# Optimization experiments

Hardware: AMD Instinct MI355X
Metric: run time of the kernel (lower is better)

The kernel has to match this reference:

```python
import jax, jax.numpy as jnp
import numpy as np
from jax import lax

BETA = 0.1

def setup_inputs() -> dict:
    key = jax.random.key(0)
    k = jax.random.split(key, 6)
    B, T, H, V = 2, 1024, 1024, 64000
    return {
        "_input": jax.random.normal(k[0], (B, T, H), jnp.float32) * 0.02,
        "weight": jax.random.normal(k[1], (V, H), jnp.float32) * 0.02,
        "attention_mask": (jax.random.uniform(k[2], (B, T)) < 0.9).astype(jnp.float32),
        "rewards": jax.random.normal(k[3], (B,), jnp.float32),
        "ref_input": jax.random.normal(k[4], (B, T, H), jnp.float32) * 0.02,
        "ref_weight": jax.random.normal(k[5], (V, H), jnp.float32) * 0.02,
    }


def _grpo(log_probs, attention_mask, rewards, ref_log_probs, beta):
    # log_probs: [B,T,V]
    chosen = jnp.argmax(log_probs, axis=-1)  # [B,T] int
    tok_lp = jnp.take_along_axis(log_probs, chosen[..., None], axis=-1)[..., 0]  # [B,T]
    ref_tok_lp = lax.stop_gradient(
        jnp.take_along_axis(ref_log_probs, chosen[..., None], axis=-1)[..., 0]
    )
    adv = (rewards - rewards.mean()) / (jnp.std(rewards, ddof=1) + 1e-8)  # [B]
    ratio = jnp.exp(tok_lp - lax.stop_gradient(tok_lp))  # == 1 in fwd, grad-carrying
    policy_loss = -ratio * adv[:, None]
    d = ref_tok_lp - tok_lp
    kl = jnp.exp(d) - d - 1.0
    per_tok = (policy_loss + beta * kl) * attention_mask
    seqlen = jnp.clip(attention_mask.sum(axis=1), 1.0)
    loss = (per_tok.sum(axis=1) / seqlen).mean()
    metrics = (
        tok_lp.mean(),
        jnp.std(tok_lp, ddof=1),
        log_probs.mean(),
        (kl * attention_mask).sum(axis=1).mean() / attention_mask.sum(axis=1).mean(),
    )
    return loss, metrics


def reference(_input, weight, attention_mask, rewards, ref_input, ref_weight):
    logits = jnp.einsum("bth,vh->btv", _input, weight)
    log_probs = jax.nn.log_softmax(logits, axis=-1)
    ref_logits = jnp.einsum("bth,vh->btv", ref_input, ref_weight)
    ref_log_probs = lax.stop_gradient(jax.nn.log_softmax(ref_logits, axis=-1))
    loss, metrics = _grpo(log_probs, attention_mask, rewards, ref_log_probs, BETA)
    return (loss, *metrics)
```

## Files before the change

### kernel.cpp

```cpp
#include <hip/hip_runtime.h>
#include <math.h>

#define GRPO_BETA 0.1f

constexpr int BM = 128;
constexpr int BN = 256;

typedef __attribute__((ext_vector_type(4))) float   f32x4;
typedef __attribute__((ext_vector_type(8))) __bf16  bf16x8;

__device__ __forceinline__ float sexp_fast(float a) { return __expf(fminf(a, 0.f)); }
__device__ __forceinline__ float sexp(float a)      { return expf(fminf(a, 0.f)); }

__device__ __forceinline__ bf16x8 cvt8(float4 a, float4 b) {
  bf16x8 r;
  r[0] = (__bf16)a.x; r[1] = (__bf16)a.y; r[2] = (__bf16)a.z; r[3] = (__bf16)a.w;
  r[4] = (__bf16)b.x; r[5] = (__bf16)b.y; r[6] = (__bf16)b.z; r[7] = (__bf16)b.w;
  return r;
}

__device__ __forceinline__ void bar_lgkm() {
  asm volatile("s_waitcnt lgkmcnt(0)\n\ts_barrier" ::: "memory");
}

__device__ __forceinline__ void gload_lds16(const void* g, void* l) {
  __builtin_amdgcn_global_load_lds(
      (const __attribute__((address_space(1))) void*)g,
      (__attribute__((address_space(3))) void*)l, 16, 0, 0);
}

__global__ __launch_bounds__(256)
void cvt_bf16_kernel(const float* __restrict__ src, __bf16* __restrict__ dst,
                     long long n8)
{
  long long i = (long long)blockIdx.x * blockDim.x + threadIdx.x;
  const long long stride = (long long)gridDim.x * blockDim.x;
  for (; i < n8; i += stride) {
    const float4 a = *reinterpret_cast<const float4*>(src + i * 8);
    const float4 b = *reinterpret_cast<const float4*>(src + i * 8 + 4);
    *reinterpret_cast<bf16x8*>(dst + i * 8) = cvt8(a, b);
  }
}

template <bool CVT, bool FULL>
__global__ __launch_bounds__(512, 4)
void fused_gemm_reduce(const float* __restrict__ AfP, const float* __restrict__ WfP,
                       const float* __restrict__ AfR, const float* __restrict__ WfR,
                       const __bf16* __restrict__ AhP, const __bf16* __restrict__ WhP,
                       const __bf16* __restrict__ AhR, const __bf16* __restrict__ WhR,
                       float* __restrict__ partP, float* __restrict__ partR,
                       int M, int K, int V, int NC, int NL, int gx)
{
  __shared__ __align__(16) unsigned short lds_a[BM * 64];
  __shared__ __align__(16) unsigned short lds_w[BN * 64];
  __shared__ __align__(16) float4 lds_red[BM * 4];

  const int tid  = threadIdx.x;
  const int lane = tid & 63;
  const int wave = tid >> 6;
  const int wm   = wave >> 2;
  const int wn   = wave & 3;
  const int l15  = lane & 15;
  const int q    = lane >> 4;

  const int nb  = gridDim.x;
  int wl = blockIdx.x;
  if ((nb & 7) == 0) wl = (wl & 7) * (nb >> 3) + (wl >> 3);
  const bool isPol = (wl & 1) == 0;
  const int  w2    = wl >> 1;
  const int  bx    = w2 % gx;
  const int  chunk = w2 / gx;
  const int  row0  = bx * BM;

  const float*  Af = isPol ? AfP : AfR;
  const float*  Wf = isPol ? WfP : WfR;
  const __bf16* Ah = isPol ? AhP : AhR;
  const __bf16* Wh = isPol ? WhP : WhR;

  const int rsub = lane >> 3;
  const int srcg = ((lane & 7) ^ rsub) * 8;

  const int t3 = tid & 3;
  const int r4 = tid >> 2;
  const int stw = ((t3 * 16) ^ ((r4 & 7) << 4));
  const int sta = r4 * 128 + stw;
  const int aroF = min(row0 + r4, M - 1) * K + t3 * 8;

  const int swzr  = ((q * 16) ^ ((l15 & 7) << 4));
  const int aoff0 = (wm * 64 + l15) * 128 + swzr;
  const int woff0 = (wn * 64 + l15) * 128 + swzr;

  float rm = -INFINITY, rse = 0.f, rsum = 0.f;
  int   ridx = 0x7fffffff;

  for (int sub = 0; sub < NL; ++sub) {
    const int v0 = (chunk * NL + sub) * BN;
    if (v0 >= V) break;

    f32x4 acc[4][4];
#pragma unroll
    for (int i = 0; i < 4; ++i)
#pragma unroll
      for (int j = 0; j < 4; ++j) acc[i][j] = (f32x4){0.f, 0.f, 0.f, 0.f};

    if constexpr (!CVT) {
      const __bf16* asrc[2];
#pragma unroll
      for (int c = 0; c < 2; ++c) {
        const int r = (wave + c * 8) * 8 + rsub;
        asrc[c] = Ah + (size_t)min(row0 + r, M - 1) * K + srcg;
      }
      const __bf16* wsrc[4];
#pragma unroll
      for (int c = 0; c < 4; ++c) {
        const int r = (wave + c * 8) * 8 + rsub;
        wsrc[c] = Wh + (size_t)min(v0 + r, V - 1) * K + srcg;
      }

      for (int kt = 0; kt < K; kt += 64) {
        __syncthreads();
#pragma unroll
        for (int c = 0; c < 2; ++c)
          gload_lds16(asrc[c] + kt,
                      reinterpret_cast<char*>(lds_a) + (wave + c * 8) * 1024);
#pragma unroll
        for (int c = 0; c < 4; ++c)
          gload_lds16(wsrc[c] + kt,
                      reinterpret_cast<char*>(lds_w) + (wave + c * 8) * 1024);
        __syncthreads();

#pragma unroll
        for (int kh = 0; kh < 2; ++kh) {
          const int p = kh << 6;
          bf16x8 afr[4];
#pragma unroll
          for (int f = 0; f < 4; ++f)
            afr[f] = *reinterpret_cast<const bf16x8*>(
                reinterpret_cast<const char*>(lds_a) + (aoff0 ^ p) + f * 2048);
          __builtin_amdgcn_s_setprio(1);
#pragma unroll
          for (int fn = 0; fn < 4; ++fn) {
            bf16x8 wfr = *reinterpret_cast<const bf16x8*>(
                reinterpret_cast<const char*>(lds_w) + (woff0 ^ p) + fn * 2048);
#pragma unroll
            for (int fm = 0; fm < 4; ++fm)
              acc[fm][fn] = __builtin_amdgcn_mfma_f32_16x16x32_bf16(
                  afr[fm], wfr, acc[fm][fn], 0, 0, 0);
          }
          __builtin_amdgcn_s_setprio(0);
        }
      }
      __syncthreads();
    } else {
      const int NS = K / 32;
      int wro[2];
#pragma unroll
      for (int i = 0; i < 2; ++i)
        wro[i] = min(v0 + r4 + 128 * i, V - 1) * K + t3 * 8;

      float4 aF[2], wF[2][2];
      aF[0] = *reinterpret_cast<const float4*>(Af + aroF);
      aF[1] = *reinterpret_cast<const float4*>(Af + aroF + 4);
#pragma unroll
      for (int i = 0; i < 2; ++i) {
        wF[i][0] = *reinterpret_cast<const float4*>(Wf + wro[i]);
        wF[i][1] = *reinterpret_cast<const float4*>(Wf + wro[i] + 4);
      }
      *reinterpret_cast<bf16x8*>(reinterpret_cast<char*>(lds_a) + sta) = cvt8(aF[0], aF[1]);
#pragma unroll
      for (int i = 0; i < 2; ++i)
        *reinterpret_cast<bf16x8*>(reinterpret_cast<char*>(lds_w) + (r4 + 128 * i) * 128 + stw) =
            cvt8(wF[i][0], wF[i][1]);
      if (NS > 1) {
        aF[0] = *reinterpret_cast<const float4*>(Af + aroF + 32);
        aF[1] = *reinterpret_cast<const float4*>(Af + aroF + 32 + 4);
#pragma unroll
        for (int i = 0; i < 2; ++i) {
          wF[i][0] = *reinterpret_cast<const float4*>(Wf + wro[i] + 32);
          wF[i][1] = *reinterpret_cast<const float4*>(Wf + wro[i] + 32 + 4);
        }
      }
      bar_lgkm();

      for (int s = 0; s < NS; ++s) {
        const int p = (s & 1) << 6;
        bf16x8 afr[4];
#pragma unroll
        for (int f = 0; f < 4; ++f)
          afr[f] = *reinterpret_cast<const bf16x8*>(
              reinterpret_cast<const char*>(lds_a) + (aoff0 ^ p) + f * 2048);
        __builtin_amdgcn_s_setprio(1);
#pragma unroll
        for (int fn = 0; fn < 4; ++fn) {
          bf16x8 wfr = *reinterpret_cast<const bf16x8*>(
              reinterpret_cast<const char*>(lds_w) + (woff0 ^ p) + fn * 2048);
#pragma unroll
          for (int fm = 0; fm < 4; ++fm)
            acc[fm][fn] = __builtin_amdgcn_mfma_f32_16x16x32_bf16(
                afr[fm], wfr, acc[fm][fn], 0, 0, 0);
        }
        __builtin_amdgcn_s_setprio(0);

        if (s + 1 < NS) {
          const int p1 = ((s + 1) & 1) << 6;
          *reinterpret_cast<bf16x8*>(reinterpret_cast<char*>(lds_a) + (sta ^ p1)) =
              cvt8(aF[0], aF[1]);
#pragma unroll
          for (int i = 0; i < 2; ++i)
            *reinterpret_cast<bf16x8*>(
                reinterpret_cast<char*>(lds_w) + (((r4 + 128 * i) * 128 + stw) ^ p1)) =
                cvt8(wF[i][0], wF[i][1]);
          if (s + 2 < NS) {
            const int kf = (s + 2) * 32;
            aF[0] = *reinterpret_cast<const float4*>(Af + aroF + kf);
            aF[1] = *reinterpret_cast<const float4*>(Af + aroF + kf + 4);
#pragma unroll
            for (int i = 0; i < 2; ++i) {
              wF[i][0] = *reinterpret_cast<const float4*>(Wf + wro[i] + kf);
              wF[i][1] = *reinterpret_cast<const float4*>(Wf + wro[i] + kf + 4);
            }
          }
        }
        bar_lgkm();
      }
    }

#pragma unroll
    for (int fm = 0; fm < 4; ++fm) {
#pragma unroll
      for (int reg = 0; reg < 4; ++reg) {
        float lm = -INFINITY;
#pragma unroll
        for (int fn = 0; fn < 4; ++fn) {
          if (FULL || v0 + wn * 64 + fn * 16 + l15 < V)
            lm = fmaxf(lm, acc[fm][fn][reg]);
        }
#pragma unroll
        for (int d = 1; d < 16; d <<= 1) lm = fmaxf(lm, __shfl_xor(lm, d));
        float se = 0.f, sm = 0.f; int li = 0x7fffffff;
#pragma unroll
        for (int fn = 0; fn < 4; ++fn) {
          const int v = v0 + wn * 64 + fn * 16 + l15;
          if (FULL || v < V) {
            const float x = acc[fm][fn][reg];
            se += __expf(x - lm);
            if (isPol) {
              sm += x;
              if (x == lm) li = min(li, v);
            }
          }
        }
        if (isPol) {
#pragma unroll
          for (int d = 1; d < 16; d <<= 1) {
            se += __shfl_xor(se, d);
            sm += __shfl_xor(sm, d);
            li  = min(li, __shfl_xor(li, d));
          }
        } else {
#pragma unroll
          for (int d = 1; d < 16; d <<= 1) se += __shfl_xor(se, d);
        }
        if (l15 == 0) {
          const int row = wm * 64 + fm * 16 + q * 4 + reg;
          lds_red[row * 4 + wn] = make_float4(lm, se, sm, __int_as_float(li));
        }
      }
    }
    __syncthreads();

    if (tid < BM) {
      float4 p0 = lds_red[tid * 4];
      float m = p0.x, se = p0.y, sm = p0.z; int idx = __float_as_int(p0.w);
#pragma unroll
      for (int j = 1; j < 4; ++j) {
        const float4 t = lds_red[tid * 4 + j];
        const int ti = __float_as_int(t.w);
        const float nm = fmaxf(m, t.x);
        se = se * sexp_fast(m - nm) + t.y * sexp_fast(t.x - nm);
        if (isPol) {
          sm += t.z;
          if (t.x > m || (t.x == m && ti < idx)) idx = ti;
        }
        m = nm;
      }
      const float nm = fmaxf(rm, m);
      rse = rse * sexp_fast(rm - nm) + se * sexp_fast(m - nm);
      if (isPol) {
        rsum += sm;
        if (m > rm || (m == rm && idx < ridx)) ridx = idx;
      }
      rm = nm;
    }
    __syncthreads();
  }

  if (tid < BM) {
    const int row = row0 + tid;
    if (row < M) {
      if (isPol) {
        reinterpret_cast<float4*>(partP)[(size_t)row * NC + chunk] =
            make_float4(rm, rse, rsum, __int_as_float(ridx));
      } else {
        reinterpret_cast<float2*>(partR)[(size_t)row * NC + chunk] =
            make_float2(rm, rse);
      }
    }
  }
}

__global__ __launch_bounds__(256)
void combine_kernel(const float4* __restrict__ partP,
                    const float2* __restrict__ partR,
                    const float* __restrict__ refA,
                    const float* __restrict__ refW,
                    float4* __restrict__ rowtab,
                    int M, int K, int V, int NC)
{
  const int row = blockIdx.x;
  const int tid = threadIdx.x;

  __shared__ float redf[256];
  __shared__ int   redi[256];
  __shared__ float s_M, s_SE, s_SUM, s_Mr, s_SEr, s_dot;
  __shared__ int   s_idx;

  float m = -INFINITY, se = 0.f, sm = 0.f; int idx = 0x7fffffff;
  for (int i = tid; i < NC; i += 256) {
    float4 p = partP[(size_t)row * NC + i];
    int pi = __float_as_int(p.w);
    float nm = fmaxf(m, p.x);
    se = se * sexp(m - nm) + p.y * sexp(p.x - nm);
    if (p.x > m || (p.x == m && pi < idx)) idx = pi;
    m = nm;
    sm += p.z;
  }
  redf[tid] = m; redi[tid] = idx;
  __syncthreads();
  for (int s = 128; s > 0; s >>= 1) {
    if (tid < s) {
      float om = redf[tid + s]; int oi = redi[tid + s];
      if (om > redf[tid] || (om == redf[tid] && oi < redi[tid])) { redf[tid] = om; redi[tid] = oi; }
    }
    __syncthreads();
  }
  if (tid == 0) { s_M = redf[0]; s_idx = redi[0]; }
  __syncthreads();
  const float Mp = s_M; const int chosen = s_idx;

  float contrib = se * sexp(m - Mp);
  __syncthreads();
  redf[tid] = contrib; __syncthreads();
  for (int s = 128; s > 0; s >>= 1) { if (tid < s) redf[tid] += redf[tid + s]; __syncthreads(); }
  if (tid == 0) s_SE = redf[0];
  __syncthreads();
  redf[tid] = sm; __syncthreads();
  for (int s = 128; s > 0; s >>= 1) { if (tid < s) redf[tid] += redf[tid + s]; __syncthreads(); }
  if (tid == 0) s_SUM = redf[0];
  __syncthreads();

  float mr = -INFINITY, ser = 0.f;
  for (int i = tid; i < NC; i += 256) {
    float2 p = partR[(size_t)row * NC + i];
    float nm = fmaxf(mr, p.x);
    ser = ser * sexp(mr - nm) + p.y * sexp(p.x - nm);
    mr = nm;
  }
  redf[tid] = mr; __syncthreads();
  for (int s = 128; s > 0; s >>= 1) { if (tid < s) redf[tid] = fmaxf(redf[tid], redf[tid + s]); __syncthreads(); }
  if (tid == 0) s_Mr = redf[0];
  __syncthreads();
  const float Mr = s_Mr;
  float contribr = ser * sexp(mr - Mr);
  __syncthreads();
  redf[tid] = contribr; __syncthreads();
  for (int s = 128; s > 0; s >>= 1) { if (tid < s) redf[tid] += redf[tid + s]; __syncthreads(); }
  if (tid == 0) s_SEr = redf[0];
  __syncthreads();

  float dp = 0.f;
  const float* ar = refA + (size_t)row * K;
  const float* wr = refW + (size_t)chosen * K;
  for (int j = tid * 4; j < K; j += 256 * 4) {
    float4 x = *reinterpret_cast<const float4*>(ar + j);
    float4 y = *reinterpret_cast<const float4*>(wr + j);
    dp = fmaf(x.x, y.x, dp);
    dp = fmaf(x.y, y.y, dp);
    dp = fmaf(x.z, y.z, dp);
    dp = fmaf(x.w, y.w, dp);
  }
  __syncthreads();
  redf[tid] = dp; __syncthreads();
  for (int s = 128; s > 0; s >>= 1) { if (tid < s) redf[tid] += redf[tid + s]; __syncthreads(); }
  if (tid == 0) s_dot = redf[0];
  __syncthreads();

  if (tid == 0) {
    float lse     = Mp + logf(s_SE);
    float tok     = Mp - lse;
    float ref_lse = Mr + logf(s_SEr);
    float ref_tok = s_dot - ref_lse;
    float d  = ref_tok - tok;
    float kl = expm1f(d) - d;
    float rm3 = s_SUM / (float)V - lse;
    rowtab[row] = make_float4(tok, kl, rm3, 0.f);
  }
}

__global__ __launch_bounds__(256)
void final_kernel(const float4* __restrict__ rowtab,
                  const float* __restrict__ mask,
                  const float* __restrict__ rewards,
                  float* __restrict__ out,
                  int M, int B, int T)
{
  const int tid = threadIdx.x;
  __shared__ float redf[256];
  __shared__ float s_mean, s_m3, s_var;
  __shared__ float s_kl[16], s_cnt[16];

  float st = 0.f, sm3 = 0.f;
  for (int r = tid; r < M; r += 256) {
    float4 v = rowtab[r];
    st += v.x; sm3 += v.z;
  }
  redf[tid] = st; __syncthreads();
  for (int s = 128; s > 0; s >>= 1) { if (tid < s) redf[tid] += redf[tid + s]; __syncthreads(); }
  if (tid == 0) s_mean = redf[0] / (float)M;
  __syncthreads();
  redf[tid] = sm3; __syncthreads();
  for (int s = 128; s > 0; s >>= 1) { if (tid < s) redf[tid] += redf[tid + s]; __syncthreads(); }
  if (tid == 0) s_m3 = redf[0] / (float)M;
  __syncthreads();

  const float mean = s_mean;
  float sv = 0.f;
  for (int r = tid; r < M; r += 256) { float d = rowtab[r].x - mean; sv = fmaf(d, d, sv); }
  __syncthreads();
  redf[tid] = sv; __syncthreads();
  for (int s = 128; s > 0; s >>= 1) { if (tid < s) redf[tid] += redf[tid + s]; __syncthreads(); }
  if (tid == 0) s_var = redf[0];
  __syncthreads();

  const int nb = B < 16 ? B : 16;
  for (int b = 0; b < nb; ++b) {
    float lk = 0.f, lc = 0.f;
    for (int t = tid; t < T; t += 256) {
      int r = b * T + t;
      float mk = mask[r];
      lk = fmaf(rowtab[r].y, mk, lk);
      lc += mk;
    }
    __syncthreads();
    redf[tid] = lk; __syncthreads();
    for (int s = 128; s > 0; s >>= 1) { if (tid < s) redf[tid] += redf[tid + s]; __syncthreads(); }
    if (tid == 0) s_kl[b] = redf[0];
    __syncthreads();
    redf[tid] = lc; __syncthreads();
    for (int s = 128; s > 0; s >>= 1) { if (tid < s) redf[tid] += redf[tid + s]; __syncthreads(); }
    if (tid == 0) s_cnt[b] = redf[0];
    __syncthreads();
  }

  if (tid == 0) {
    float rmean = 0.f;
    for (int b = 0; b < B; ++b) rmean += rewards[b];
    rmean /= (float)B;
    float rv = 0.f;
    for (int b = 0; b < B; ++b) { float d = rewards[b] - rmean; rv += d * d; }
    float rstd = sqrtf(rv / (float)(B > 1 ? B - 1 : 1));

    float loss = 0.f, m4n = 0.f, m4d = 0.f;
    for (int b = 0; b < nb; ++b) {
      float adv  = (rewards[b] - rmean) / (rstd + 1e-8f);
      float cnt  = s_cnt[b];
      float seql = fmaxf(cnt, 1.0f);
      loss += (-adv * cnt + GRPO_BETA * s_kl[b]) / seql;
      m4n += s_kl[b];
      m4d += cnt;
    }
    loss /= (float)B;

    out[0] = loss;
    out[1] = s_mean;
    out[2] = sqrtf(s_var / (float)(M - 1));
    out[3] = s_m3;
    out[4] = m4n / m4d;
  }
}

extern "C" void kernel_launch(void* const* d_in, const int* in_sizes, int n_in,
                              void* d_out, int out_size, void* d_ws, size_t ws_size,
                              hipStream_t stream)
{
  if (n_in < 6) return;
  const float* A       = (const float*)d_in[0];
  const float* W       = (const float*)d_in[1];
  const float* mask    = (const float*)d_in[2];
  const float* rewards = (const float*)d_in[3];
  const float* rA      = (const float*)d_in[4];
  const float* rW      = (const float*)d_in[5];

  const int M = in_sizes[2];
  const int B = in_sizes[3];
  const int T = M / B;
  const int K = in_sizes[0] / M;
  const int V = in_sizes[1] / K;

  const int gx = (M + BM - 1) / BM;
  const bool full = (V % BN) == 0;

  const size_t aBytes = (size_t)M * K * sizeof(__bf16);
  const size_t wBytes = (size_t)V * K * sizeof(__bf16);
  auto partBytes = [&](int nl) -> size_t {
    int nc = (V + BN * nl - 1) / (BN * nl);
    return (size_t)M * nc * 16 + (size_t)M * nc * 8 + (size_t)M * 16;
  };

  int NL = 1;
  bool canPrep = false;
  if (K % 64 == 0) {
    for (int nl = 1; nl <= 1024; nl <<= 1) {
      size_t pb = (partBytes(nl) + 255) & ~(size_t)255;
      if (pb + 2 * aBytes + 2 * wBytes <= ws_size) { NL = nl; canPrep = true; break; }
    }
  }
  if (!canPrep) {
    NL = 1;
    while (partBytes(NL) > ws_size && NL < 1024) NL <<= 1;
  }
  const int NC = (V + BN * NL - 1) / (BN * NL);

  float* partP  = (float*)d_ws;
  float* partR  = partP + (size_t)M * NC * 4;
  float* rowtab = partR + (size_t)M * NC * 2;

  dim3 g1(2 * gx * NC), b1(512);

  if (canPrep) {
    size_t pb = (partBytes(NL) + 255) & ~(size_t)255;
    __bf16* Ab  = (__bf16*)((char*)d_ws + pb);
    __bf16* rAb = Ab  + (size_t)M * K;
    __bf16* Wb  = rAb + (size_t)M * K;
    __bf16* rWb = Wb  + (size_t)V * K;

    const long long nA8 = (long long)M * K / 8;
    const long long nW8 = (long long)V * K / 8;
    cvt_bf16_kernel<<<dim3(512),  dim3(256), 0, stream>>>(A,  Ab,  nA8);
    cvt_bf16_kernel<<<dim3(512),  dim3(256), 0, stream>>>(rA, rAb, nA8);
    cvt_bf16_kernel<<<dim3(2048), dim3(256), 0, stream>>>(W,  Wb,  nW8);
    cvt_bf16_kernel<<<dim3(2048), dim3(256), 0, stream>>>(rW, rWb, nW8);

    if (full) {
      fused_gemm_reduce<false, true ><<<g1, b1, 0, stream>>>(
          nullptr, nullptr, nullptr, nullptr, Ab, Wb, rAb, rWb,
          partP, partR, M, K, V, NC, NL, gx);
    } else {
      fused_gemm_reduce<false, false><<<g1, b1, 0, stream>>>(
          nullptr, nullptr, nullptr, nullptr, Ab, Wb, rAb, rWb,
          partP, partR, M, K, V, NC, NL, gx);
    }
  } else {
    if (full) {
      fused_gemm_reduce<true , true ><<<g1, b1, 0, stream>>>(
          A, W, rA, rW, nullptr, nullptr, nullptr, nullptr,
          partP, partR, M, K, V, NC, NL, gx);
    } else {
      fused_gemm_reduce<true , false><<<g1, b1, 0, stream>>>(
          A, W, rA, rW, nullptr, nullptr, nullptr, nullptr,
          partP, partR, M, K, V, NC, NL, gx);
    }
  }

  combine_kernel<<<dim3(M), dim3(256), 0, stream>>>(
      (const float4*)partP, (const float2*)partR, rA, rW, (float4*)rowtab, M, K, V, NC);
  final_kernel<<<dim3(1), dim3(256), 0, stream>>>(
      (const float4*)rowtab, mask, rewards, (float*)d_out, M, B, T);
}
```

Measured before the change: 877.8 us.

## Double-buffer LDS tiles with async global-to-LDS loads across K=32 steps

```diff
diff --git a/kernel.cpp b/kernel.cpp
--- a/kernel.cpp
+++ b/kernel.cpp
@@ -77,15 +77,22 @@
   const __bf16* Ah = isPol ? AhP : AhR;
   const __bf16* Wh = isPol ? WhP : WhR;
 
-  const int rsub = lane >> 3;
-  const int srcg = ((lane & 7) ^ rsub) * 8;
+  const int lrow = lane >> 2;
+  const int gsw  = ((lane & 3) ^ (lrow & 3)) * 8;
+  const __bf16* asrc = Ah ? Ah + (size_t)min(row0 + wave * 16 + lrow, M - 1) * K + gsw : nullptr;
+  char* adst = reinterpret_cast<char*>(lds_a) + wave * 1024;
+  char* wdst0 = reinterpret_cast<char*>(lds_w) + wave * 1024;
+  char* wdst1 = reinterpret_cast<char*>(lds_w) + (wave + 8) * 1024;
+
+  const int rswz   = ((q ^ (l15 & 3)) << 4);
+  const int a32off = (wm * 64 + l15) * 64 + rswz;
+  const int w32off = (wn * 64 + l15) * 64 + rswz;
 
   const int t3 = tid & 3;
   const int r4 = tid >> 2;
   const int stw = ((t3 * 16) ^ ((r4 & 7) << 4));
   const int sta = r4 * 128 + stw;
   const int aroF = min(row0 + r4, M - 1) * K + t3 * 8;
-
   const int swzr  = ((q * 16) ^ ((l15 & 7) << 4));
   const int aoff0 = (wm * 64 + l15) * 128 + swzr;
   const int woff0 = (wn * 64 + l15) * 128 + swzr;
@@ -104,53 +111,52 @@
       for (int j = 0; j < 4; ++j) acc[i][j] = (f32x4){0.f, 0.f, 0.f, 0.f};
 
     if constexpr (!CVT) {
-      const __bf16* asrc[2];
-#pragma unroll
-      for (int c = 0; c < 2; ++c) {
-        const int r = (wave + c * 8) * 8 + rsub;
-        asrc[c] = Ah + (size_t)min(row0 + r, M - 1) * K + srcg;
-      }
-      const __bf16* wsrc[4];
-#pragma unroll
-      for (int c = 0; c < 4; ++c) {
-        const int r = (wave + c * 8) * 8 + rsub;
-        wsrc[c] = Wh + (size_t)min(v0 + r, V - 1) * K + srcg;
-      }
-
-      for (int kt = 0; kt < K; kt += 64) {
-        __syncthreads();
-#pragma unroll
-        for (int c = 0; c < 2; ++c)
-          gload_lds16(asrc[c] + kt,
-                      reinterpret_cast<char*>(lds_a) + (wave + c * 8) * 1024);
-#pragma unroll
-        for (int c = 0; c < 4; ++c)
-          gload_lds16(wsrc[c] + kt,
-                      reinterpret_cast<char*>(lds_w) + (wave + c * 8) * 1024);
-        __syncthreads();
-
-#pragma unroll
-        for (int kh = 0; kh < 2; ++kh) {
-          const int p = kh << 6;
-          bf16x8 afr[4];
-#pragma unroll
-          for (int f = 0; f < 4; ++f)
-            afr[f] = *reinterpret_cast<const bf16x8*>(
-                reinterpret_cast<const char*>(lds_a) + (aoff0 ^ p) + f * 2048);
-          __builtin_amdgcn_s_setprio(1);
-#pragma unroll
-          for (int fn = 0; fn < 4; ++fn) {
-            bf16x8 wfr = *reinterpret_cast<const bf16x8*>(
-                reinterpret_cast<const char*>(lds_w) + (woff0 ^ p) + fn * 2048);
-#pragma unroll
-            for (int fm = 0; fm < 4; ++fm)
-              acc[fm][fn] = __builtin_amdgcn_mfma_f32_16x16x32_bf16(
-                  afr[fm], wfr, acc[fm][fn], 0, 0, 0);
-          }
-          __builtin_amdgcn_s_setprio(0);
-        }
-      }
-      __syncthreads();
+      const __bf16* wsrc0 = Wh + (size_t)min(v0 + wave * 16 + lrow, V - 1) * K + gsw;
+      const __bf16* wsrc1 = Wh + (size_t)min(v0 + (wave + 8) * 16 + lrow, V - 1) * K + gsw;
+      const int NT = K / 32;
+
+      gload_lds16(asrc,            adst);
+      gload_lds16(wsrc0,           wdst0);
+      gload_lds16(wsrc1,           wdst1);
+      if (NT > 1) {
+        gload_lds16(asrc  + 32,    adst  + 8192);
+        gload_lds16(wsrc0 + 32,    wdst0 + 16384);
+        gload_lds16(wsrc1 + 32,    wdst1 + 16384);
+      }
+
+      for (int t = 0; t < NT; ++t) {
+        if (t + 1 < NT) asm volatile("s_waitcnt vmcnt(3)" ::: "memory");
+        else            asm volatile("s_waitcnt vmcnt(0)" ::: "memory");
+        __builtin_amdgcn_s_barrier();
+
+        const int pa = (t & 1) << 13;
+        const int pw = (t & 1) << 14;
+        bf16x8 afr[4];
+#pragma unroll
+        for (int f = 0; f < 4; ++f)
+          afr[f] = *reinterpret_cast<const bf16x8*>(
+              reinterpret_cast<const char*>(lds_a) + pa + a32off + f * 1024);
+        __builtin_amdgcn_s_setprio(1);
+#pragma unroll
+        for (int fn = 0; fn < 4; ++fn) {
+          bf16x8 wfr = *reinterpret_cast<const bf16x8*>(
+              reinterpret_cast<const char*>(lds_w) + pw + w32off + fn * 1024);
+#pragma unroll
+          for (int fm = 0; fm < 4; ++fm)
+            acc[fm][fn] = __builtin_amdgcn_mfma_f32_16x16x32_bf16(
+                afr[fm], wfr, acc[fm][fn], 0, 0, 0);
+        }
+        __builtin_amdgcn_s_setprio(0);
+
+        __builtin_amdgcn_s_barrier();
+        asm volatile("" ::: "memory");
+        if (t + 2 < NT) {
+          const size_t ko = (size_t)(t + 2) * 32;
+          gload_lds16(asrc  + ko, adst  + pa);
+          gload_lds16(wsrc0 + ko, wdst0 + pw);
+          gload_lds16(wsrc1 + ko, wdst1 + pw);
+        }
+      }
     } else {
       const int NS = K / 32;
       int wro[2];
@@ -519,7 +525,7 @@
 
   int NL = 1;
   bool canPrep = false;
-  if (K % 64 == 0) {
+  if (K % 32 == 0 && K >= 64) {
     for (int nl = 1; nl <= 1024; nl <<= 1) {
       size_t pb = (partBytes(nl) + 255) & ~(size_t)255;
       if (pb + 2 * aBytes + 2 * wBytes <= ws_size) { NL = nl; canPrep = true; break; }
```

After: 925.1 us. 1.05x slower.
